# Optimization experiments

Measured on AMD Instinct MI355X. Metric: run time of the kernel, lower is better.

## Reference

```python
import jax, jax.numpy as jnp
import numpy as np

L, D, H, HD, I, V = 22, 768, 12, 64, 1152, 50368
B, S = 8, 1024
EPS = 1e-5
WIN = 128  # local attention window (total width)
NEG = -1e9


def _ln(x, w):
    m = jnp.mean(x, -1, keepdims=True)
    v = jnp.var(x, -1, keepdims=True)
    return (x - m) * jax.lax.rsqrt(v + EPS) * w


def _rope_tables(theta, s):
    inv = 1.0 / (theta ** (jnp.arange(0, HD, 2, dtype=jnp.float32) / HD))
    f = jnp.arange(s, dtype=jnp.float32)[:, None] * inv[None, :]
    emb = jnp.concatenate([f, f], -1)  # [S, HD]
    return jnp.cos(emb), jnp.sin(emb)


def _rot_half(x):
    x1, x2 = x[..., :HD // 2], x[..., HD // 2:]
    return jnp.concatenate([-x2, x1], -1)


def setup_inputs() -> dict:
    key = jax.random.key(0)
    ks = jax.random.split(key, 8)
    sc = 0.02
    return {
        'input_ids': jax.random.randint(ks[0], (B, S), 0, V),
        'attention_mask': jnp.ones((B, S), dtype=jnp.int32),
        'tok_emb': jax.random.normal(ks[1], (V, D), dtype=jnp.float32) * sc,
        'emb_norm_w': jnp.ones((D,), jnp.float32),
        'attn_norm_w': jnp.ones((L, D), jnp.float32),
        'Wqkv': jax.random.normal(ks[2], (L, D, 3 * D), dtype=jnp.float32) * sc,
        'Wo': jax.random.normal(ks[3], (L, D, D), dtype=jnp.float32) * sc,
        'mlp_norm_w': jnp.ones((L, D), jnp.float32),
        'Wi': jax.random.normal(ks[4], (L, D, 2 * I), dtype=jnp.float32) * sc,
        'Wmo': jax.random.normal(ks[5], (L, I, D), dtype=jnp.float32) * sc,
        'final_norm_w': jnp.ones((D,), jnp.float32),
        'cls_w': jax.random.normal(ks[6], (D, 1), dtype=jnp.float32) * sc,
        'cls_b': jnp.zeros((1,), jnp.float32),
    }


def reference(input_ids, attention_mask, tok_emb, emb_norm_w, attn_norm_w, Wqkv,
              Wo, mlp_norm_w, Wi, Wmo, final_norm_w, cls_w, cls_b):
    b, s = input_ids.shape
    x = _ln(tok_emb[input_ids], emb_norm_w)  # [B,S,D]
    pad_ok = attention_mask.astype(bool)[:, None, None, :]  # [B,1,1,S]
    pos = jnp.arange(s)
    local_ok = jnp.abs(pos[:, None] - pos[None, :]) <= WIN // 2  # [S,S]
    glob_mask = jnp.where(pad_ok, 0.0, NEG)
    loc_mask = jnp.where(pad_ok & local_ok[None, None], 0.0, NEG)
    cos_g, sin_g = _rope_tables(160000.0, s)
    cos_l, sin_l = _rope_tables(10000.0, s)
    scale = 1.0 / jnp.sqrt(jnp.float32(HD))
    for l in range(L):
        is_global = (l % 3 == 0)
        h = x if l == 0 else _ln(x, attn_norm_w[l])
        qkv = (h @ Wqkv[l]).reshape(b, s, 3, H, HD)
        q = jnp.transpose(qkv[:, :, 0], (0, 2, 1, 3))  # [B,H,S,hd]
        k = jnp.transpose(qkv[:, :, 1], (0, 2, 1, 3))
        v = jnp.transpose(qkv[:, :, 2], (0, 2, 1, 3))
        cos, sin = (cos_g, sin_g) if is_global else (cos_l, sin_l)
        q = q * cos + _rot_half(q) * sin
        k = k * cos + _rot_half(k) * sin
        scores = jnp.einsum('bhqd,bhkd->bhqk', q, k) * scale
        scores = scores + (glob_mask if is_global else loc_mask)
        attn = jax.nn.softmax(scores, -1) @ v  # [B,H,S,hd]
        attn = jnp.transpose(attn, (0, 2, 1, 3)).reshape(b, s, D)
        x = x + attn @ Wo[l]
        hm = _ln(x, mlp_norm_w[l])
        a = hm @ Wi[l]
        inp_a, gate = a[..., :I], a[..., I:]
        x = x + (jax.nn.gelu(inp_a, approximate=False) * gate) @ Wmo[l]
    x = _ln(x, final_norm_w)
    m = attention_mask[..., None].astype(x.dtype)
    pooled = jnp.sum(x * m, axis=1) / jnp.clip(jnp.sum(m, axis=1), 1e-9)
    logits = pooled @ cls_w + cls_b  # [B,1]
    scores_out = jax.nn.sigmoid(logits)[:, 0]  # [B]
    return scores_out, logits
```

## Files before the change

kernel.cpp:

```cpp
#include <hip/hip_runtime.h>

typedef unsigned short u16;
typedef __attribute__((ext_vector_type(8))) short short8;
typedef __attribute__((ext_vector_type(8))) unsigned short u16x8;
typedef __attribute__((ext_vector_type(4))) unsigned short u16x4;
typedef __attribute__((ext_vector_type(4))) float floatx4;
typedef __attribute__((ext_vector_type(2))) unsigned uint2v;

#define L_LAYERS 22
#define D_MODEL 768
#define N_HEADS 12
#define HEAD_D 64
#define I_FF 1152
#define B_BATCH 8
#define S_SEQ 1024
#define M_ROWS (B_BATCH * S_SEQ)

__device__ __forceinline__ u16 f2bf(float f) {
    union { float f; unsigned u; } v; v.f = f;
    unsigned r = v.u + 0x7fffu + ((v.u >> 16) & 1u);
    return (u16)(r >> 16);
}
__device__ __forceinline__ float bf2f(u16 u) {
    union { unsigned u; float f; } v; v.u = ((unsigned)u) << 16;
    return v.f;
}
__device__ __forceinline__ unsigned cvtpk(float lo, float hi) {
    unsigned r;
    asm("v_cvt_pk_bf16_f32 %0, %1, %2" : "=v"(r) : "v"(lo), "v"(hi));
    return r;
}
__device__ __forceinline__ void gload16(const u16* g, u16* l) {
    __builtin_amdgcn_global_load_lds(
        (const __attribute__((address_space(1))) unsigned int*)g,
        (__attribute__((address_space(3))) unsigned int*)l,
        16, 0, 0);
}

__global__ __launch_bounds__(256) void rope_tables_kernel(float* cg, float* sg, float* cl, float* sl) {
    int i = blockIdx.x * 256 + threadIdx.x;
    if (i >= 1024 * 32) return;
    int s = i >> 5, j = i & 31;
    float e = (float)(2 * j) / 64.f;
    float fg = (float)s * powf(160000.f, -e);
    float fl = (float)s * powf(10000.f, -e);
    cg[i] = cosf(fg); sg[i] = sinf(fg);
    cl[i] = cosf(fl); sl[i] = sinf(fl);
}

__global__ __launch_bounds__(256) void embed_ln_kernel(const int* __restrict__ ids,
                                                       const float* __restrict__ emb,
                                                       const float* __restrict__ w,
                                                       u16* __restrict__ x,
                                                       u16* __restrict__ hbf) {
    int tok = blockIdx.x;
    int tid = threadIdx.x;
    const float* row = emb + (size_t)ids[tok] * D_MODEL;
    float v[3]; float s = 0.f, q = 0.f;
#pragma unroll
    for (int i = 0; i < 3; ++i) { v[i] = row[tid + 256 * i]; s += v[i]; q += v[i] * v[i]; }
#pragma unroll
    for (int o = 32; o; o >>= 1) { s += __shfl_down(s, o); q += __shfl_down(q, o); }
    __shared__ float rs[4], rq[4];
    int wid = tid >> 6, lane = tid & 63;
    if (!lane) { rs[wid] = s; rq[wid] = q; }
    __syncthreads();
    s = rs[0] + rs[1] + rs[2] + rs[3]; q = rq[0] + rq[1] + rq[2] + rq[3];
    float mean = s * (1.f / 768.f);
    float var = q * (1.f / 768.f) - mean * mean;
    float rstd = rsqrtf(var + 1e-5f);
#pragma unroll
    for (int i = 0; i < 3; ++i) {
        u16 y = f2bf((v[i] - mean) * rstd * w[tid + 256 * i]);
        x[(size_t)tok * D_MODEL + tid + 256 * i] = y;
        hbf[(size_t)tok * D_MODEL + tid + 256 * i] = y;
    }
}

__global__ __launch_bounds__(256) void ln4_kernel(const u16* __restrict__ x,
                                                  const float* __restrict__ w,
                                                  u16* __restrict__ out_bf) {
    int row = blockIdx.x * 4 + (threadIdx.x >> 6);
    int lane = threadIdx.x & 63;
    const u16* p = x + (size_t)row * D_MODEL + lane * 4;
    float v[12];
    float s = 0.f, q = 0.f;
#pragma unroll
    for (int i = 0; i < 3; ++i) {
        u16x4 t = *(const u16x4*)(p + i * 256);
#pragma unroll
        for (int j = 0; j < 4; ++j) {
            float f = bf2f(t[j]);
            v[i * 4 + j] = f; s += f; q += f * f;
        }
    }
#pragma unroll
    for (int o = 32; o; o >>= 1) { s += __shfl_xor(s, o); q += __shfl_xor(q, o); }
    float mean = s * (1.f / 768.f);
    float var = q * (1.f / 768.f) - mean * mean;
    float rstd = rsqrtf(var + 1e-5f);
#pragma unroll
    for (int i = 0; i < 3; ++i) {
        floatx4 wv = *(const floatx4*)(w + i * 256 + lane * 4);
        u16x4 pk = { f2bf((v[i * 4 + 0] - mean) * rstd * wv[0]),
                     f2bf((v[i * 4 + 1] - mean) * rstd * wv[1]),
                     f2bf((v[i * 4 + 2] - mean) * rstd * wv[2]),
                     f2bf((v[i * 4 + 3] - mean) * rstd * wv[3]) };
        *(u16x4*)(out_bf + (size_t)row * D_MODEL + i * 256 + lane * 4) = pk;
    }
}

__global__ __launch_bounds__(256) void stats_kernel(const u16* __restrict__ x,
                                                    float* __restrict__ st) {
    int row = blockIdx.x * 4 + (threadIdx.x >> 6);
    int lane = threadIdx.x & 63;
    const u16* p = x + (size_t)row * D_MODEL + lane * 4;
    float s = 0.f, q = 0.f;
#pragma unroll
    for (int i = 0; i < 3; ++i) {
        u16x4 t = *(const u16x4*)(p + i * 256);
#pragma unroll
        for (int j = 0; j < 4; ++j) { float f = bf2f(t[j]); s += f; q += f * f; }
    }
#pragma unroll
    for (int o = 32; o; o >>= 1) { s += __shfl_xor(s, o); q += __shfl_xor(q, o); }
    if (!lane) {
        float mean = s * (1.f / 768.f);
        float var = q * (1.f / 768.f) - mean * mean;
        st[row * 2] = mean;
        st[row * 2 + 1] = rsqrtf(var + 1e-5f);
    }
}

__global__ __launch_bounds__(256) void weight_prep_kernel(const float* __restrict__ W,
                                                          u16* __restrict__ out,
                                                          int Kw, int Nw, int perm,
                                                          long in_ls, long out_ls) {
    __shared__ float tile[32][33];
    int l = blockIdx.z;
    const float* in = W + (size_t)l * in_ls;
    u16* o = out + (size_t)l * out_ls;
    int c0 = blockIdx.x * 32, r0 = blockIdx.y * 32;
    int tc = threadIdx.x & 31, tr = threadIdx.x >> 5;
#pragma unroll
    for (int i = 0; i < 4; ++i) {
        int r = tr + i * 8;
        tile[r][tc] = in[(size_t)(r0 + r) * Nw + c0 + tc];
    }
    __syncthreads();
#pragma unroll
    for (int i = 0; i < 4; ++i) {
        int cc = c0 + tr + i * 8;
        int prow = cc;
        if (perm) {
            if (cc < 1152) prow = ((cc >> 4) << 5) + (cc & 15);
            else { int j = cc - 1152; prow = ((j >> 4) << 5) + 16 + (j & 15); }
        }
        o[(size_t)prow * Kw + r0 + tc] = f2bf(tile[tc][tr + i * 8]);
    }
}

#define GEMM_CORE(A_, B_, K_)                                                     \
    int tid = threadIdx.x;                                                        \
    int lane = tid & 63, wid = tid >> 6;                                          \
    int uw = __builtin_amdgcn_readfirstlane(wid);                                 \
    int lr = lane & 15, lg = lane >> 4;                                           \
    int nwg = gridDim.x * gridDim.y;                                              \
    int orig = blockIdx.y * gridDim.x + blockIdx.x;                               \
    int cpx = nwg >> 3;                                                           \
    int nb = (orig & 7) * cpx + (orig >> 3);                                      \
    int bn = (nb % gridDim.x) * 128, bm = (nb / gridDim.x) * 128;                 \
    int wr = (wid >> 1) * 64, wc = (wid & 1) * 64;                                \
    floatx4 acc[4][4] = {};                                                       \
    int srow = lane >> 3;                                                         \
    int sg8 = ((lane & 7) ^ srow) * 8;                                            \
    const u16* Abase = A_ + (size_t)(bm + uw * 8 + srow) * K_ + sg8;              \
    const u16* Bbase = B_ + (size_t)(bn + uw * 8 + srow) * K_ + sg8;              \
    for (int k0 = 0; k0 < K_; k0 += 64) {                                         \
        __syncthreads();                                                          \
        _Pragma("unroll")                                                         \
        for (int i = 0; i < 4; ++i) {                                             \
            gload16(Abase + (size_t)(i * 32) * K_ + k0, As + (uw * 8 + i * 32) * 64); \
            gload16(Bbase + (size_t)(i * 32) * K_ + k0, Bs + (uw * 8 + i * 32) * 64); \
        }                                                                         \
        __syncthreads();                                                          \
        short8 af[4][2], bfr[4][2];                                               \
        _Pragma("unroll")                                                         \
        for (int t = 0; t < 4; ++t) {                                             \
            int ra = (wr + t * 16 + lr) * 64, rb = (wc + t * 16 + lr) * 64;       \
            int x7 = (lr & 7);                                                    \
            af[t][0]  = *(const short8*)&As[ra + ((lg ^ x7) << 3)];               \
            af[t][1]  = *(const short8*)&As[ra + (((4 + lg) ^ x7) << 3)];         \
            bfr[t][0] = *(const short8*)&Bs[rb + ((lg ^ x7) << 3)];               \
            bfr[t][1] = *(const short8*)&Bs[rb + (((4 + lg) ^ x7) << 3)];         \
        }                                                                         \
        __builtin_amdgcn_s_setprio(1);                                            \
        _Pragma("unroll")                                                         \
        for (int mi = 0; mi < 4; ++mi)                                            \
            _Pragma("unroll")                                                     \
            for (int ni = 0; ni < 4; ++ni) {                                      \
                acc[mi][ni] = __builtin_amdgcn_mfma_f32_16x16x32_bf16(af[mi][0], bfr[ni][0], acc[mi][ni], 0, 0, 0); \
                acc[mi][ni] = __builtin_amdgcn_mfma_f32_16x16x32_bf16(af[mi][1], bfr[ni][1], acc[mi][ni], 0, 0, 0); \
            }                                                                     \
        __builtin_amdgcn_s_setprio(0);                                            \
    }

__global__ __launch_bounds__(256) void gemm64_kernel(const u16* __restrict__ A,
                                                     const u16* __restrict__ B,
                                                     const u16* __restrict__ R,
                                                     u16* __restrict__ C,
                                                     int M, int N, int K) {
    __shared__ u16 As[64 * 64];
    __shared__ u16 Bs[128 * 64];
    int tid = threadIdx.x;
    int lane = tid & 63, wid = tid >> 6;
    int uw = __builtin_amdgcn_readfirstlane(wid);
    int lr = lane & 15, lg = lane >> 4;
    int nwg = gridDim.x * gridDim.y;
    int orig = blockIdx.y * gridDim.x + blockIdx.x;
    int cpx = nwg >> 3;
    int nb = (orig & 7) * cpx + (orig >> 3);
    int bn = (nb % gridDim.x) * 128, bm = (nb / gridDim.x) * 64;
    int wr = (wid >> 1) * 32, wc = (wid & 1) * 64;
    floatx4 acc[2][4] = {};
    int srow = lane >> 3;
    int sg8 = ((lane & 7) ^ srow) * 8;
    const u16* Abase = A + (size_t)(bm + uw * 16 + srow) * K + sg8;
    const u16* Bbase = B + (size_t)(bn + uw * 32 + srow) * K + sg8;
    for (int k0 = 0; k0 < K; k0 += 64) {
        __syncthreads();
#pragma unroll
        for (int i = 0; i < 2; ++i)
            gload16(Abase + (size_t)(i * 8) * K + k0, As + (uw * 16 + i * 8) * 64);
#pragma unroll
        for (int i = 0; i < 4; ++i)
            gload16(Bbase + (size_t)(i * 8) * K + k0, Bs + (uw * 32 + i * 8) * 64);
        __syncthreads();
        short8 af[2][2], bfr[4][2];
        int x7 = (lr & 7);
#pragma unroll
        for (int t = 0; t < 2; ++t) {
            int ra = (wr + t * 16 + lr) * 64;
            af[t][0] = *(const short8*)&As[ra + ((lg ^ x7) << 3)];
            af[t][1] = *(const short8*)&As[ra + (((4 + lg) ^ x7) << 3)];
        }
#pragma unroll
        for (int t = 0; t < 4; ++t) {
            int rb = (wc + t * 16 + lr) * 64;
            bfr[t][0] = *(const short8*)&Bs[rb + ((lg ^ x7) << 3)];
            bfr[t][1] = *(const short8*)&Bs[rb + (((4 + lg) ^ x7) << 3)];
        }
        __builtin_amdgcn_s_setprio(1);
#pragma unroll
        for (int mi = 0; mi < 2; ++mi)
#pragma unroll
            for (int ni = 0; ni < 4; ++ni) {
                acc[mi][ni] = __builtin_amdgcn_mfma_f32_16x16x32_bf16(af[mi][0], bfr[ni][0], acc[mi][ni], 0, 0, 0);
                acc[mi][ni] = __builtin_amdgcn_mfma_f32_16x16x32_bf16(af[mi][1], bfr[ni][1], acc[mi][ni], 0, 0, 0);
            }
        __builtin_amdgcn_s_setprio(0);
    }
#pragma unroll
    for (int mi = 0; mi < 2; ++mi) {
        int m = bm + wr + mi * 16 + lg * 4;
#pragma unroll
        for (int ni = 0; ni < 4; ++ni) {
            int n = bn + wc + ni * 16 + lr;
#pragma unroll
            for (int r = 0; r < 4; ++r) {
                size_t idx = (size_t)(m + r) * N + n;
                C[idx] = f2bf(acc[mi][ni][r] + bf2f(R[idx]));
            }
        }
    }
}

template<int MODE>
__global__ __launch_bounds__(256) void gemm_nt_kernel(const u16* __restrict__ A,
                                                      const u16* __restrict__ B,
                                                      void* __restrict__ Cout,
                                                      int M, int N, int K,
                                                      const float* __restrict__ cosT,
                                                      const float* __restrict__ sinT,
                                                      u16* __restrict__ Qo,
                                                      u16* __restrict__ Ko,
                                                      u16* __restrict__ Vt) {
    __shared__ u16 smem[16384];
    u16* As = smem;
    u16* Bs = smem + 8192;
    GEMM_CORE(A, B, K)

    if constexpr (MODE == 2) {
        int nbc = bn + wc;
        int which = nbc / 768;
        int h = (nbc - which * 768) >> 6;
        if (which < 2) {
            u16* Out = which ? Ko : Qo;
#pragma unroll
            for (int mi = 0; mi < 4; ++mi)
#pragma unroll
                for (int r = 0; r < 4; ++r) {
                    int m = bm + wr + mi * 16 + lg * 4 + r;
                    int s = m & 1023, b = m >> 10;
                    size_t base = ((size_t)(b * N_HEADS + h) * S_SEQ + s) * HEAD_D;
#pragma unroll
                    for (int ni = 0; ni < 2; ++ni) {
                        int j = ni * 16 + lr;
                        float c = cosT[s * 32 + j], sn = sinT[s * 32 + j];
                        float q1 = acc[mi][ni][r], q2 = acc[mi][ni + 2][r];
                        Out[base + j]      = f2bf(q1 * c - q2 * sn);
                        Out[base + j + 32] = f2bf(q2 * c + q1 * sn);
                    }
                }
        } else {
            __syncthreads();
#pragma unroll
            for (int mi = 0; mi < 4; ++mi)
#pragma unroll
                for (int ni = 0; ni < 4; ++ni) {
                    int dloc = wc + ni * 16 + lr;
                    int mloc = wr + mi * 16 + lg * 4;
                    int pu = (mloc >> 2) ^ ((dloc & 7) << 2);
                    u16x4 pk = { f2bf(acc[mi][ni][0]), f2bf(acc[mi][ni][1]),
                                 f2bf(acc[mi][ni][2]), f2bf(acc[mi][ni][3]) };
                    *(u16x4*)&smem[dloc * 128 + pu * 4] = pk;
                }
            __syncthreads();
            int b = bm >> 10, s0 = bm & 1023;
            int h0b = (bn - 1536) >> 6;
            int d = tid >> 1, sh = (tid & 1) * 64;
            int bh = b * N_HEADS + h0b + (d >> 6);
            u16* dst = Vt + ((size_t)bh * HEAD_D + (d & 63)) * S_SEQ + s0 + sh;
#pragma unroll
            for (int jj = 0; jj < 8; ++jj) {
                int u0 = (((sh + jj * 8) >> 2) ^ ((d & 7) << 2));
                *(u16x8*)(dst + jj * 8) = *(const u16x8*)&smem[d * 128 + u0 * 4];
            }
        }
    }
    if constexpr (MODE == 3) {
        int t0 = (bn + wc) >> 5;
#pragma unroll
        for (int mi = 0; mi < 4; ++mi)
#pragma unroll
            for (int r = 0; r < 4; ++r) {
                int m = bm + wr + mi * 16 + lg * 4 + r;
#pragma unroll
                for (int p = 0; p < 2; ++p) {
                    float vi = acc[mi][2 * p][r];
                    float vg = acc[mi][2 * p + 1][r];
                    float ge = 0.5f * vi * (1.f + erff(vi * 0.70710678118654752f));
                    ((u16*)Cout)[(size_t)m * I_FF + (t0 + p) * 16 + lr] = f2bf(ge * vg);
                }
            }
    }
}

template<int IS_LOCAL>
__global__ __launch_bounds__(256) void flash_attn_kernel(const u16* __restrict__ Q,
                                                         const u16* __restrict__ Kb,
                                                         const u16* __restrict__ Vt,
                                                         u16* __restrict__ O) {
    __shared__ u16 Ks[64][72];
    __shared__ u16 Vs[64][72];
    __shared__ u16 Pl[4][16][72];
    const float C1 = 0.18033688011112042f;
    int bh = blockIdx.y;
    int b = bh / 12, h = bh - b * 12;
    int qb0 = blockIdx.x * 64;
    int tid = threadIdx.x, lane = tid & 63, wid = tid >> 6;
    int lr = lane & 15, lg = lane >> 4;
    int q_row = qb0 + wid * 16 + lr;
    const u16* Qrow = Q + ((size_t)bh * S_SEQ + q_row) * HEAD_D + lg * 8;
    short8 qf0 = *(const short8*)Qrow;
    short8 qf1 = *(const short8*)(Qrow + 32);
    floatx4 accO[4] = {};
    float m_run = -1e30f, l_run = 0.f;
    int kstart = 0, kend = S_SEQ;
    if (IS_LOCAL) {
        kstart = qb0 >= 64 ? qb0 - 64 : 0;
        kend = qb0 + 128 > S_SEQ ? S_SEQ : qb0 + 128;
    }
    int nt = (kend - kstart) >> 6;
    u16x8 kreg[2], vreg[2];
    int su_r = tid >> 3, su_c = (tid & 7) * 8;
    int su_r2 = (tid + 256) >> 3;
    {
        int k0 = kstart;
        kreg[0] = *(const u16x8*)(Kb + ((size_t)bh * S_SEQ + k0 + su_r) * HEAD_D + su_c);
        vreg[0] = *(const u16x8*)(Vt + ((size_t)bh * HEAD_D + su_r) * S_SEQ + k0 + su_c);
        kreg[1] = *(const u16x8*)(Kb + ((size_t)bh * S_SEQ + k0 + su_r2) * HEAD_D + su_c);
        vreg[1] = *(const u16x8*)(Vt + ((size_t)bh * HEAD_D + su_r2) * S_SEQ + k0 + su_c);
    }
    for (int t = 0; t < nt; ++t) {
        int k0 = kstart + (t << 6);
        if (t) __syncthreads();
        *(u16x8*)&Ks[su_r][su_c]  = kreg[0];
        *(u16x8*)&Vs[su_r][su_c]  = vreg[0];
        *(u16x8*)&Ks[su_r2][su_c] = kreg[1];
        *(u16x8*)&Vs[su_r2][su_c] = vreg[1];
        if (t + 1 < nt) {
            int kn = k0 + 64;
            kreg[0] = *(const u16x8*)(Kb + ((size_t)bh * S_SEQ + kn + su_r) * HEAD_D + su_c);
            vreg[0] = *(const u16x8*)(Vt + ((size_t)bh * HEAD_D + su_r) * S_SEQ + kn + su_c);
            kreg[1] = *(const u16x8*)(Kb + ((size_t)bh * S_SEQ + kn + su_r2) * HEAD_D + su_c);
            vreg[1] = *(const u16x8*)(Vt + ((size_t)bh * HEAD_D + su_r2) * S_SEQ + kn + su_c);
        }
        __syncthreads();
        float sv[16]; float mloc = -1e30f;
        __builtin_amdgcn_s_setprio(1);
#pragma unroll
        for (int g = 0; g < 4; ++g) {
            short8 kf0 = *(const short8*)&Ks[g * 16 + lr][lg * 8];
            short8 kf1 = *(const short8*)&Ks[g * 16 + lr][lg * 8 + 32];
            floatx4 sg0 = {};
            sg0 = __builtin_amdgcn_mfma_f32_16x16x32_bf16(kf0, qf0, sg0, 0, 0, 0);
            sg0 = __builtin_amdgcn_mfma_f32_16x16x32_bf16(kf1, qf1, sg0, 0, 0, 0);
#pragma unroll
            for (int r = 0; r < 4; ++r) {
                float s1 = sg0[r];
                if (IS_LOCAL) {
                    int kpos = k0 + g * 16 + lg * 4 + r;
                    int dd = q_row - kpos; if (dd < 0) dd = -dd;
                    if (dd > 64) s1 = -1e9f;
                }
                sv[g * 4 + r] = s1; mloc = fmaxf(mloc, s1);
            }
        }
        __builtin_amdgcn_s_setprio(0);
        mloc = fmaxf(mloc, __shfl_xor(mloc, 16));
        mloc = fmaxf(mloc, __shfl_xor(mloc, 32));
        if (!__all(mloc - m_run <= 64.f)) {
            float m_new = fmaxf(m_run, mloc);
            float alpha = exp2f((m_run - m_new) * C1);
            l_run *= alpha;
#pragma unroll
            for (int c = 0; c < 4; ++c)
#pragma unroll
                for (int r = 0; r < 4; ++r) accO[c][r] *= alpha;
            m_run = m_new;
        }
        float mc = m_run * C1;
        float pv[16]; float psum = 0.f;
#pragma unroll
        for (int i = 0; i < 16; ++i) {
            pv[i] = exp2f(sv[i] * C1 - mc);
            psum += pv[i];
        }
        psum += __shfl_xor(psum, 16);
        psum += __shfl_xor(psum, 32);
        l_run += psum;
#pragma unroll
        for (int g = 0; g < 4; ++g) {
            uint2v w = { cvtpk(pv[g * 4], pv[g * 4 + 1]), cvtpk(pv[g * 4 + 2], pv[g * 4 + 3]) };
            *(uint2v*)&Pl[wid][lr][g * 16 + lg * 4] = w;
        }
        asm volatile("s_waitcnt lgkmcnt(0)" ::: "memory");
        __builtin_amdgcn_sched_barrier(0);
        short8 pf0 = *(const short8*)&Pl[wid][lr][lg * 8];
        short8 pf1 = *(const short8*)&Pl[wid][lr][32 + lg * 8];
        __builtin_amdgcn_s_setprio(1);
#pragma unroll
        for (int c = 0; c < 4; ++c) {
            short8 vf0 = *(const short8*)&Vs[c * 16 + lr][lg * 8];
            short8 vf1 = *(const short8*)&Vs[c * 16 + lr][lg * 8 + 32];
            accO[c] = __builtin_amdgcn_mfma_f32_16x16x32_bf16(vf0, pf0, accO[c], 0, 0, 0);
            accO[c] = __builtin_amdgcn_mfma_f32_16x16x32_bf16(vf1, pf1, accO[c], 0, 0, 0);
        }
        __builtin_amdgcn_s_setprio(0);
    }
    float inv_l = 1.0f / l_run;
#pragma unroll
    for (int c = 0; c < 4; ++c) {
        uint2v pk = { cvtpk(accO[c][0] * inv_l, accO[c][1] * inv_l),
                      cvtpk(accO[c][2] * inv_l, accO[c][3] * inv_l) };
        *(uint2v*)&Pl[wid][lr][c * 16 + lg * 4] = pk;
    }
    asm volatile("s_waitcnt lgkmcnt(0)" ::: "memory");
    __builtin_amdgcn_sched_barrier(0);
    int orow = lane & 15, part = lane >> 4;
    u16* dst = O + ((size_t)b * S_SEQ + qb0 + wid * 16 + orow) * D_MODEL + h * 64 + part * 16;
    *(u16x8*)dst       = *(const u16x8*)&Pl[wid][orow][part * 16];
    *(u16x8*)(dst + 8) = *(const u16x8*)&Pl[wid][orow][part * 16 + 8];
}

__global__ __launch_bounds__(256) void pool1_kernel(const u16* __restrict__ x,
                                                    const float* __restrict__ st,
                                                    const int* __restrict__ amask,
                                                    float* __restrict__ partial) {
    int ch = blockIdx.x, b = blockIdx.y;
    int s0 = ch * 64;
    float a0 = 0.f, a1 = 0.f, a2 = 0.f;
    for (int i = 0; i < 64; ++i) {
        int s = s0 + i;
        int row = b * S_SEQ + s;
        float m = (float)amask[row];
        float mean = st[row * 2], rstd = st[row * 2 + 1];
        const u16* p = x + (size_t)row * D_MODEL;
        a0 += (bf2f(p[threadIdx.x])       - mean) * rstd * m;
        a1 += (bf2f(p[threadIdx.x + 256]) - mean) * rstd * m;
        a2 += (bf2f(p[threadIdx.x + 512]) - mean) * rstd * m;
    }
    float* dst = partial + ((size_t)(b * 16 + ch)) * D_MODEL;
    dst[threadIdx.x] = a0; dst[threadIdx.x + 256] = a1; dst[threadIdx.x + 512] = a2;
}

__global__ __launch_bounds__(256) void pool2_kernel(const float* __restrict__ partial,
                                                    float* __restrict__ pooledsum) {
#pragma unroll
    for (int j = 0; j < 3; ++j) {
        int d = threadIdx.x + j * 256;
        float a = 0.f;
        for (int ch = 0; ch < 16; ++ch)
            a += partial[((size_t)(blockIdx.x * 16 + ch)) * D_MODEL + d];
        pooledsum[blockIdx.x * D_MODEL + d] = a;
    }
}

__global__ __launch_bounds__(256) void logits_kernel(const float* __restrict__ pooledsum,
                                                     const int* __restrict__ amask,
                                                     const float* __restrict__ fin_w,
                                                     const float* __restrict__ cls_w,
                                                     const float* __restrict__ cls_b,
                                                     float* __restrict__ out) {
    int b = blockIdx.x;
    float p = 0.f, cnt = 0.f;
    for (int d = threadIdx.x; d < D_MODEL; d += 256)
        p += pooledsum[b * D_MODEL + d] * fin_w[d] * cls_w[d];
    for (int s = threadIdx.x; s < S_SEQ; s += 256) cnt += (float)amask[b * S_SEQ + s];
#pragma unroll
    for (int o = 32; o; o >>= 1) { p += __shfl_down(p, o); cnt += __shfl_down(cnt, o); }
    __shared__ float rp[4], rc[4];
    int wid = threadIdx.x >> 6, lane = threadIdx.x & 63;
    if (!lane) { rp[wid] = p; rc[wid] = cnt; }
    __syncthreads();
    if (threadIdx.x == 0) {
        float pt = rp[0] + rp[1] + rp[2] + rp[3];
        float ct = rc[0] + rc[1] + rc[2] + rc[3];
        float l = pt / fmaxf(ct, 1e-9f) + cls_b[0];
        out[b] = 1.f / (1.f + expf(-l));
        out[8 + b] = l;
    }
}

extern "C" void kernel_launch(void* const* d_in, const int* in_sizes, int n_in,
                              void* d_out, int out_size, void* d_ws, size_t ws_size,
                              hipStream_t stream) {
    const int*   ids     = (const int*)d_in[0];
    const int*   amask   = (const int*)d_in[1];
    const float* tok_emb = (const float*)d_in[2];
    const float* emb_w   = (const float*)d_in[3];
    const float* attn_w  = (const float*)d_in[4];
    const float* Wqkv    = (const float*)d_in[5];
    const float* Wo      = (const float*)d_in[6];
    const float* mlp_w   = (const float*)d_in[7];
    const float* Wi      = (const float*)d_in[8];
    const float* Wmo     = (const float*)d_in[9];
    const float* fin_w   = (const float*)d_in[10];
    const float* cls_w   = (const float*)d_in[11];
    const float* cls_b   = (const float*)d_in[12];
    float* out = (float*)d_out;

    char* wsp = (char*)d_ws;
    size_t off = 0;
    auto alloc = [&](size_t bytes) -> void* {
        void* p = wsp + off;
        off = (off + bytes + 255) & ~(size_t)255;
        return p;
    };
    u16*   x      = (u16*)  alloc((size_t)M_ROWS * D_MODEL * 2);
    u16*   hbf    = (u16*)  alloc((size_t)M_ROWS * D_MODEL * 2);
    u16*   Qb     = (u16*)  alloc((size_t)96 * S_SEQ * HEAD_D * 2);
    u16*   Kbuf   = (u16*)  alloc((size_t)96 * S_SEQ * HEAD_D * 2);
    u16*   Vt     = (u16*)  alloc((size_t)96 * HEAD_D * S_SEQ * 2);
    u16*   act2   = (u16*)  alloc((size_t)M_ROWS * I_FF * 2);
    u16*   qkvT   = (u16*)  alloc((size_t)L_LAYERS * 2304 * 768 * 2);
    u16*   woT    = (u16*)  alloc((size_t)L_LAYERS * 768 * 768 * 2);
    u16*   wiT    = (u16*)  alloc((size_t)L_LAYERS * 2304 * 768 * 2);
    u16*   wmoT   = (u16*)  alloc((size_t)L_LAYERS * 768 * 1152 * 2);
    float* st     = (float*)alloc((size_t)M_ROWS * 2 * 4);
    float* tabs   = (float*)alloc((size_t)4 * 1024 * 32 * 4);
    float* partial= (float*)alloc((size_t)8 * 16 * D_MODEL * 4);
    float* pooled = (float*)alloc((size_t)8 * D_MODEL * 4);
    float* cg = tabs, *sg = tabs + 32768, *cl = tabs + 65536, *sl = tabs + 98304;

    rope_tables_kernel<<<128, 256, 0, stream>>>(cg, sg, cl, sl);
    weight_prep_kernel<<<dim3(72, 24, L_LAYERS), 256, 0, stream>>>(
        Wqkv, qkvT, 768, 2304, 0, 768L * 2304, 2304L * 768);
    weight_prep_kernel<<<dim3(24, 24, L_LAYERS), 256, 0, stream>>>(
        Wo, woT, 768, 768, 0, 768L * 768, 768L * 768);
    weight_prep_kernel<<<dim3(72, 24, L_LAYERS), 256, 0, stream>>>(
        Wi, wiT, 768, 2304, 1, 768L * 2304, 2304L * 768);
    weight_prep_kernel<<<dim3(24, 36, L_LAYERS), 256, 0, stream>>>(
        Wmo, wmoT, 1152, 768, 0, 1152L * 768, 768L * 1152);
    embed_ln_kernel<<<M_ROWS, 256, 0, stream>>>(ids, tok_emb, emb_w, x, hbf);

    for (int l = 0; l < L_LAYERS; ++l) {
        int is_global = (l % 3) == 0;
        const float* cosT = is_global ? cg : cl;
        const float* sinT = is_global ? sg : sl;
        u16* qkvTl = qkvT + (size_t)l * 2304 * 768;
        u16* woTl  = woT  + (size_t)l * 768 * 768;
        u16* wiTl  = wiT  + (size_t)l * 2304 * 768;
        u16* wmoTl = wmoT + (size_t)l * 768 * 1152;
        if (l > 0)
            ln4_kernel<<<M_ROWS / 4, 256, 0, stream>>>(x, attn_w + (size_t)l * 768, hbf);
        gemm_nt_kernel<2><<<dim3(2304 / 128, M_ROWS / 128), 256, 0, stream>>>(
            hbf, qkvTl, nullptr, M_ROWS, 2304, 768, cosT, sinT, Qb, Kbuf, Vt);
        if (is_global)
            flash_attn_kernel<0><<<dim3(16, 96), 256, 0, stream>>>(Qb, Kbuf, Vt, act2);
        else
            flash_attn_kernel<1><<<dim3(16, 96), 256, 0, stream>>>(Qb, Kbuf, Vt, act2);
        gemm64_kernel<<<dim3(768 / 128, M_ROWS / 64), 256, 0, stream>>>(
            act2, woTl, x, x, M_ROWS, 768, 768);
        ln4_kernel<<<M_ROWS / 4, 256, 0, stream>>>(x, mlp_w + (size_t)l * 768, hbf);
        gemm_nt_kernel<3><<<dim3(2304 / 128, M_ROWS / 128), 256, 0, stream>>>(
            hbf, wiTl, act2, M_ROWS, 2304, 768, nullptr, nullptr, nullptr, nullptr, nullptr);
        gemm64_kernel<<<dim3(768 / 128, M_ROWS / 64), 256, 0, stream>>>(
            act2, wmoTl, x, x, M_ROWS, 768, 1152);
    }

    stats_kernel<<<M_ROWS / 4, 256, 0, stream>>>(x, st);
    pool1_kernel<<<dim3(16, 8), 256, 0, stream>>>(x, st, amask, partial);
    pool2_kernel<<<8, 256, 0, stream>>>(partial, pooled);
    logits_kernel<<<8, 256, 0, stream>>>(pooled, amask, fin_w, cls_w, cls_b, out);
}
```

Before: 3.933 ms.

## Double-buffer GEMM LDS tiles with K=32 stages and async prefetch

Replaces the single-buffered 128x128x64 GEMM main loop with a two-stage LDS ring of K=32 tiles. The next tile is prefetched via direct global-to-LDS loads while MFMAs run on the current tile, using vmcnt waits and raw barriers. This aims to hide global load latency and remove one of the two barriers per iteration. The cost is a shorter K step, so more loop iterations and barriers per unit of work, plus a new swizzle for 32-wide rows.

New measurement: 4.154 ms. 1.06x slower.

```diff
diff --git a/kernel.cpp b/kernel.cpp
--- a/kernel.cpp
+++ b/kernel.cpp
@@ -159,51 +159,6 @@
         o[(size_t)prow * Kw + r0 + tc] = f2bf(tile[tc][tr + i * 8]);
     }
 }
-
-#define GEMM_CORE(A_, B_, K_)                                                     \
-    int tid = threadIdx.x;                                                        \
-    int lane = tid & 63, wid = tid >> 6;                                          \
-    int uw = __builtin_amdgcn_readfirstlane(wid);                                 \
-    int lr = lane & 15, lg = lane >> 4;                                           \
-    int nwg = gridDim.x * gridDim.y;                                              \
-    int orig = blockIdx.y * gridDim.x + blockIdx.x;                               \
-    int cpx = nwg >> 3;                                                           \
-    int nb = (orig & 7) * cpx + (orig >> 3);                                      \
-    int bn = (nb % gridDim.x) * 128, bm = (nb / gridDim.x) * 128;                 \
-    int wr = (wid >> 1) * 64, wc = (wid & 1) * 64;                                \
-    floatx4 acc[4][4] = {};                                                       \
-    int srow = lane >> 3;                                                         \
-    int sg8 = ((lane & 7) ^ srow) * 8;                                            \
-    const u16* Abase = A_ + (size_t)(bm + uw * 8 + srow) * K_ + sg8;              \
-    const u16* Bbase = B_ + (size_t)(bn + uw * 8 + srow) * K_ + sg8;              \
-    for (int k0 = 0; k0 < K_; k0 += 64) {                                         \
-        __syncthreads();                                                          \
-        _Pragma("unroll")                                                         \
-        for (int i = 0; i < 4; ++i) {                                             \
-            gload16(Abase + (size_t)(i * 32) * K_ + k0, As + (uw * 8 + i * 32) * 64); \
-            gload16(Bbase + (size_t)(i * 32) * K_ + k0, Bs + (uw * 8 + i * 32) * 64); \
-        }                                                                         \
-        __syncthreads();                                                          \
-        short8 af[4][2], bfr[4][2];                                               \
-        _Pragma("unroll")                                                         \
-        for (int t = 0; t < 4; ++t) {                                             \
-            int ra = (wr + t * 16 + lr) * 64, rb = (wc + t * 16 + lr) * 64;       \
-            int x7 = (lr & 7);                                                    \
-            af[t][0]  = *(const short8*)&As[ra + ((lg ^ x7) << 3)];               \
-            af[t][1]  = *(const short8*)&As[ra + (((4 + lg) ^ x7) << 3)];         \
-            bfr[t][0] = *(const short8*)&Bs[rb + ((lg ^ x7) << 3)];               \
-            bfr[t][1] = *(const short8*)&Bs[rb + (((4 + lg) ^ x7) << 3)];         \
-        }                                                                         \
-        __builtin_amdgcn_s_setprio(1);                                            \
-        _Pragma("unroll")                                                         \
-        for (int mi = 0; mi < 4; ++mi)                                            \
-            _Pragma("unroll")                                                     \
-            for (int ni = 0; ni < 4; ++ni) {                                      \
-                acc[mi][ni] = __builtin_amdgcn_mfma_f32_16x16x32_bf16(af[mi][0], bfr[ni][0], acc[mi][ni], 0, 0, 0); \
-                acc[mi][ni] = __builtin_amdgcn_mfma_f32_16x16x32_bf16(af[mi][1], bfr[ni][1], acc[mi][ni], 0, 0, 0); \
-            }                                                                     \
-        __builtin_amdgcn_s_setprio(0);                                            \
-    }
 
 __global__ __launch_bounds__(256) void gemm64_kernel(const u16* __restrict__ A,
                                                      const u16* __restrict__ B,
@@ -285,10 +240,63 @@
                                                       u16* __restrict__ Qo,
                                                       u16* __restrict__ Ko,
                                                       u16* __restrict__ Vt) {
-    __shared__ u16 smem[16384];
-    u16* As = smem;
-    u16* Bs = smem + 8192;
-    GEMM_CORE(A, B, K)
+    __shared__ u16 smem[2][2][128 * 32];
+    int tid = threadIdx.x;
+    int lane = tid & 63, wid = tid >> 6;
+    int uw = __builtin_amdgcn_readfirstlane(wid);
+    int lr = lane & 15, lg = lane >> 4;
+    int nwg = gridDim.x * gridDim.y;
+    int orig = blockIdx.y * gridDim.x + blockIdx.x;
+    int cpx = nwg >> 3;
+    int nb = (orig & 7) * cpx + (orig >> 3);
+    int bn = (nb % gridDim.x) * 128, bm = (nb / gridDim.x) * 128;
+    int wr = (wid >> 1) * 64, wc = (wid & 1) * 64;
+    floatx4 acc[4][4] = {};
+    int srow = lane >> 2, ss = lane & 3;
+    int sg8 = (ss ^ (srow & 3)) * 8;
+    const u16* Abase = A + (size_t)(bm + uw * 16 + srow) * K + sg8;
+    const u16* Bbase = B + (size_t)(bn + uw * 16 + srow) * K + sg8;
+    int NT = K >> 5;
+
+    auto stage = [&](int c, int kt) {
+        int k0 = kt << 5;
+#pragma unroll
+        for (int i = 0; i < 2; ++i) {
+            gload16(Abase + (size_t)(i * 64) * K + k0, &smem[c][0][(uw * 16 + i * 64) * 32]);
+            gload16(Bbase + (size_t)(i * 64) * K + k0, &smem[c][1][(uw * 16 + i * 64) * 32]);
+        }
+    };
+
+    stage(0, 0);
+    stage(1, 1);
+    asm volatile("s_waitcnt vmcnt(4)" ::: "memory");
+    __builtin_amdgcn_s_barrier();
+
+    for (int kt = 0; kt < NT; ++kt) {
+        int c = kt & 1;
+        short8 af[4], bfr[4];
+        int x3 = (lr & 3);
+#pragma unroll
+        for (int t = 0; t < 4; ++t) {
+            af[t]  = *(const short8*)&smem[c][0][(wr + t * 16 + lr) * 32 + ((lg ^ x3) << 3)];
+            bfr[t] = *(const short8*)&smem[c][1][(wc + t * 16 + lr) * 32 + ((lg ^ x3) << 3)];
+        }
+        __builtin_amdgcn_s_setprio(1);
+#pragma unroll
+        for (int mi = 0; mi < 4; ++mi)
+#pragma unroll
+            for (int ni = 0; ni < 4; ++ni)
+                acc[mi][ni] = __builtin_amdgcn_mfma_f32_16x16x32_bf16(af[mi], bfr[ni], acc[mi][ni], 0, 0, 0);
+        __builtin_amdgcn_s_setprio(0);
+        __builtin_amdgcn_s_barrier();
+        if (kt + 2 < NT) stage(c, kt + 2);
+        if (kt + 1 < NT) {
+            if (kt + 2 < NT) asm volatile("s_waitcnt vmcnt(4)" ::: "memory");
+            else             asm volatile("s_waitcnt vmcnt(0)" ::: "memory");
+            __builtin_amdgcn_sched_barrier(0);
+            __builtin_amdgcn_s_barrier();
+        }
+    }
 
     if constexpr (MODE == 2) {
         int nbc = bn + wc;
@@ -313,6 +321,7 @@
                     }
                 }
         } else {
+            u16* sfl = &smem[0][0][0];
             __syncthreads();
 #pragma unroll
             for (int mi = 0; mi < 4; ++mi)
@@ -323,7 +332,7 @@
                     int pu = (mloc >> 2) ^ ((dloc & 7) << 2);
                     u16x4 pk = { f2bf(acc[mi][ni][0]), f2bf(acc[mi][ni][1]),
                                  f2bf(acc[mi][ni][2]), f2bf(acc[mi][ni][3]) };
-                    *(u16x4*)&smem[dloc * 128 + pu * 4] = pk;
+                    *(u16x4*)&sfl[dloc * 128 + pu * 4] = pk;
                 }
             __syncthreads();
             int b = bm >> 10, s0 = bm & 1023;
@@ -334,7 +343,7 @@
 #pragma unroll
             for (int jj = 0; jj < 8; ++jj) {
                 int u0 = (((sh + jj * 8) >> 2) ^ ((d & 7) << 2));
-                *(u16x8*)(dst + jj * 8) = *(const u16x8*)&smem[d * 128 + u0 * 4];
+                *(u16x8*)(dst + jj * 8) = *(const u16x8*)&sfl[d * 128 + u0 * 4];
             }
         }
     }
```
